# Kernel optimization log

Hardware: AMD Instinct MI355X
Metric: run time of the kernel (lower is better)

The kernel has to match this reference:

```python
import jax, jax.numpy as jnp
import numpy as np

S, B, T, H, E, V, OOV = 400, 16, 64, 512, 256, 50000, 50


def _w(k, shape, scale=0.02):
    return scale * jax.random.normal(k, shape, dtype=jnp.float32)


def setup_inputs() -> dict:
    key = jax.random.key(0)
    ks = jax.random.split(key, 20)
    H2 = H // 2
    return {
        "inputs": jax.random.randint(ks[0], (S, B), 0, V),
        "inputs_length": jnp.full((B,), S, dtype=jnp.int32),  # full lengths (packing is then a no-op)
        "inputs_extended": jax.random.randint(ks[1], (S, B), 0, V + OOV),
        "oov_size": OOV,
        "outputs": jax.random.randint(ks[2], (T, B), 0, V),
        "embedding": _w(ks[3], (V, E)),
        "enc_Wih_f": _w(ks[4], (4 * H2, E)), "enc_Whh_f": _w(ks[5], (4 * H2, H2)),
        "enc_bih_f": jnp.zeros(4 * H2), "enc_bhh_f": jnp.zeros(4 * H2),
        "enc_Wih_b": _w(ks[6], (4 * H2, E)), "enc_Whh_b": _w(ks[7], (4 * H2, H2)),
        "enc_bih_b": jnp.zeros(4 * H2), "enc_bhh_b": jnp.zeros(4 * H2),
        "feat_W": _w(ks[8], (H, H)),
        "dec_Wih": _w(ks[9], (4 * H, E)), "dec_Whh": _w(ks[10], (4 * H, H)),
        "dec_bih": jnp.zeros(4 * H), "dec_bhh": jnp.zeros(4 * H),
        "attn_W": _w(ks[11], (H, H)),
        "vocab_W": _w(ks[12], (V, 3 * H)), "vocab_b": jnp.zeros(V),
        "ptr_W": _w(ks[13], (1, 3 * H)), "ptr_b": jnp.zeros(1),
    }


def _lstm(xs, Wih, Whh, bih, bhh, reverse=False):
    # xs: [S, B, E] -> ys [S, B, H2], final (h, c)
    Bn, H2 = xs.shape[1], Whh.shape[1]

    def step(carry, x):
        h, c = carry
        g = x @ Wih.T + bih + h @ Whh.T + bhh
        i, f, gg, o = jnp.split(g, 4, axis=-1)  # pytorch gate order i,f,g,o
        c = jax.nn.sigmoid(f) * c + jax.nn.sigmoid(i) * jnp.tanh(gg)
        h = jax.nn.sigmoid(o) * jnp.tanh(c)
        return (h, c), h

    init = (jnp.zeros((Bn, H2), xs.dtype), jnp.zeros((Bn, H2), xs.dtype))
    (h, c), ys = jax.lax.scan(step, init, xs, reverse=reverse)
    return ys, h, c


def _forward(inputs, inputs_extended, oov_size, outputs, embedding,
             enc_Wih_f, enc_Whh_f, enc_bih_f, enc_bhh_f,
             enc_Wih_b, enc_Whh_b, enc_bih_b, enc_bhh_b,
             feat_W, dec_Wih, dec_Whh, dec_bih, dec_bhh,
             attn_W, vocab_W, vocab_b, ptr_W, ptr_b):
    Hn = dec_Whh.shape[1]
    Tn, Bn = outputs.shape
    Sn = inputs.shape[0]

    x = embedding[inputs]  # [S,B,E]
    yf, hf, cf = _lstm(x, enc_Wih_f, enc_Whh_f, enc_bih_f, enc_bhh_f)
    yb, hb, cb = _lstm(x, enc_Wih_b, enc_Whh_b, enc_bih_b, enc_bhh_b, reverse=True)
    enc_seq = jnp.concatenate([yf, yb], axis=-1)              # [S,B,H]
    enc_out = jnp.transpose(enc_seq @ feat_W.T, (1, 2, 0))    # Permute(1,2,0) -> [B,H,S]
    # View(-1, H) on [2,B,H/2] stacked states (faithful reshape, incl. batch mixing)
    h0 = jnp.stack([hf, hb]).reshape(-1, Hn)                  # [B,H]
    c0 = jnp.stack([cf, cb]).reshape(-1, Hn)

    yemb = embedding[outputs]                                 # [T,B,E]
    idx = inputs_extended.T                                   # [B,S]
    rows = jnp.arange(Bn)[:, None]
    t_ids = jnp.arange(Tn)

    def step(carry, inp):
        t, xt = inp
        h, c, prev_attn, hid_buf = carry
        # LSTMCell
        g = xt @ dec_Wih.T + dec_bih + h @ dec_Whh.T + dec_bhh
        i, f, gg, o = jnp.split(g, 4, axis=-1)
        c = jax.nn.sigmoid(f) * c + jax.nn.sigmoid(i) * jnp.tanh(gg)
        h = jax.nn.sigmoid(o) * jnp.tanh(c)
        # intra-temporal attention (NB: faithful to source, the *normalized*
        # previous attention is fed back as temporal_scores_sum)
        scores = jnp.exp(jnp.einsum('bh,bhs->bs', h, enc_out))   # [B,S]
        attn = jnp.where(t == 0, scores, scores / prev_attn)
        attn = attn / attn.sum(-1, keepdims=True)                # Normalize(-1)
        enc_ctx = jnp.einsum('bs,bhs->bh', attn, enc_out)        # [B,H]
        # intra-decoder attention over previous decoder hiddens
        keys = hid_buf @ attn_W.T                                # [T,B,H]
        sc = jnp.einsum('bh,tbh->bt', h, keys)
        sc = jnp.where(t_ids[None, :] < t, sc, -1e30)
        a = jax.nn.softmax(sc, axis=-1)
        dec_ctx = jnp.where(t == 0, 0.0, jnp.einsum('bt,tbh->bh', a, hid_buf))
        hid_buf = hid_buf.at[t].set(h)
        # pointer-generator
        feats = jnp.concatenate([h, enc_ctx, dec_ctx], axis=-1)  # [B,3H]
        vdist = jax.nn.softmax(feats @ vocab_W.T + vocab_b, axis=1)
        p = jax.nn.sigmoid(feats @ ptr_W.T + ptr_b)              # [B,1]
        vdist = (1.0 - p) * vdist
        copy = p * attn                                          # [B,S]
        vpad = jnp.pad(vdist, ((0, 0), (0, oov_size)))
        final = vpad.at[rows, idx].add(copy)                     # scatter_add
        return (h, c, attn, hid_buf), final

    hid_buf0 = jnp.zeros((Tn, Bn, Hn))
    init = (h0, c0, jnp.ones((Bn, Sn)), hid_buf0)
    _, preds = jax.lax.scan(step, init, (t_ids, yemb))
    return preds  # [T, B, V+oov]


def reference(inputs, inputs_length, inputs_extended, oov_size, outputs, embedding,
              enc_Wih_f, enc_Whh_f, enc_bih_f, enc_bhh_f,
              enc_Wih_b, enc_Whh_b, enc_bih_b, enc_bhh_b,
              feat_W, dec_Wih, dec_Whh, dec_bih, dec_bhh,
              attn_W, vocab_W, vocab_b, ptr_W, ptr_b):
    # inputs_length is full-length here, so packed RNN == plain scan
    return _forward(inputs, inputs_extended, oov_size, outputs, embedding,
                    enc_Wih_f, enc_Whh_f, enc_bih_f, enc_bhh_f,
                    enc_Wih_b, enc_Whh_b, enc_bih_b, enc_bhh_b,
                    feat_W, dec_Wih, dec_Whh, dec_bih, dec_bhh,
                    attn_W, vocab_W, vocab_b, ptr_W, ptr_b)
```

## Files before the change

### kernel.cpp

```cpp
#include <hip/hip_runtime.h>
#include <cstdint>
#include <cstddef>

typedef unsigned char uchar;
typedef unsigned short ushort;
typedef unsigned int uint;
typedef unsigned long long u64;
typedef __attribute__((ext_vector_type(4))) float f32x4;
typedef __attribute__((ext_vector_type(4))) uint u32x4;
typedef __attribute__((ext_vector_type(4))) int i32x4;

#define DI __device__ __forceinline__

#define S_  400
#define B_  16
#define T_  64
#define H_  512
#define H2_ 256
#define E_  256
#define V_  50000
#define VO_ 50050
#define LP_ 50048

constexpr size_t O_WENCWIH  = 0;
constexpr size_t O_WDECWIH  = O_WENCWIH + (size_t)2048*256*2;
constexpr size_t O_WDECWHH  = O_WDECWIH + (size_t)2048*256*2;
constexpr size_t O_WFEAT    = O_WDECWHH + (size_t)2048*512*2;
constexpr size_t O_WATTN    = O_WFEAT   + (size_t)512*512*2;
constexpr size_t O_BENC     = O_WATTN   + (size_t)512*512*2;
constexpr size_t O_BDEC     = O_BENC    + 2048*4;
constexpr size_t O_WENCWHH8 = O_BDEC    + 2048*4;
constexpr size_t O_XENC     = O_WENCWHH8+ (size_t)2*1024*256;
constexpr size_t O_XDEC     = O_XENC    + (size_t)6400*256*2;
constexpr size_t O_XINENC   = O_XDEC    + (size_t)1024*256*2;
constexpr size_t O_XD       = O_XINENC  + (size_t)2*400*16*1024*2;
constexpr size_t O_ENCSEQ   = O_XD      + (size_t)64*16*2048*2;
constexpr size_t O_ENCOUT   = O_ENCSEQ  + (size_t)6400*512*2;
constexpr size_t O_HFIN     = O_ENCOUT  + (size_t)16*400*512*2;
constexpr size_t O_CFIN     = O_HFIN    + 8192*4;
constexpr size_t O_HBUF     = O_CFIN    + 8192*4;
constexpr size_t O_CSTATE   = O_HBUF    + (size_t)2*8192*2;
constexpr size_t O_HIDBUF   = O_CSTATE  + 8192*4;
constexpr size_t O_KEYS     = O_HIDBUF  + (size_t)64*8192*2;
constexpr size_t O_ATTN     = O_KEYS    + (size_t)64*8192*2;
constexpr size_t O_ATTNQ    = O_ATTN    + (size_t)64*16*400*4;
constexpr size_t O_PSUM     = O_ATTNQ   + (size_t)64*16*400*4;
constexpr size_t O_CTXSLOT  = O_PSUM    + 2*32*16*4;
constexpr size_t O_FEATS    = O_CTXSLOT + (size_t)32*16*512*4;
constexpr size_t O_P        = O_FEATS   + (size_t)1024*1536;
constexpr size_t O_INVSUM   = O_P       + 1024*4;
constexpr size_t O_VOCAB8   = O_INVSUM  + 1024*4;
constexpr size_t O_LOGITS   = O_VOCAB8  + (size_t)50048*1536;
constexpr size_t O_A16      = O_XINENC;
constexpr size_t O_ENCT     = O_A16   + (size_t)16*64*416*2;
constexpr size_t O_HIDT     = O_ENCT  + (size_t)16*512*416*2;

DI float b2f(ushort u){ uint x = ((uint)u) << 16; return __builtin_bit_cast(float, x); }
DI ushort f2b(float f){
  uint u = __builtin_bit_cast(uint, f);
  return (ushort)((u + 0x7fffu + ((u >> 16) & 1u)) >> 16);
}
DI uchar f2e4(float f){
  int q = __builtin_amdgcn_cvt_pk_fp8_f32(f, 0.f, 0, false);
  return (uchar)(q & 0xff);
}
DI uchar f2i8(float f, float scale){
  float q = rintf(f * scale);
  q = fminf(127.f, fmaxf(-127.f, q));
  return (uchar)(signed char)(int)q;
}
DI float e42f(uint b){ return __builtin_amdgcn_cvt_f32_fp8((int)b, 0); }
DI float sigm(float x){ return 1.f / (1.f + __expf(-x)); }
DI float tanhf_(float x){ return 2.f / (1.f + __expf(-2.f * x)) - 1.f; }

DI f32x4 mfma16_bf16(u32x4 a, u32x4 b, f32x4 c){
  asm("v_mfma_f32_16x16x32_bf16 %0, %1, %2, %0" : "+v"(c) : "v"(a), "v"(b));
  return c;
}
DI f32x4 mfma16_fp8(u64 a, u64 b, f32x4 c){
  asm("v_mfma_f32_16x16x32_fp8_fp8 %0, %1, %2, %0" : "+v"(c) : "v"(a), "v"(b));
  return c;
}
DI void mfma_fence(){ asm volatile("s_nop 7\n\ts_nop 7"); }
DI void barrier_lds(){ asm volatile("s_waitcnt lgkmcnt(0)\n\ts_barrier" ::: "memory"); }
DI void wait_vm0(){ asm volatile("s_waitcnt vmcnt(0)" ::: "memory"); }

DI int dot4(int a, int b, int c){
#if __has_builtin(__builtin_amdgcn_sdot4)
  return __builtin_amdgcn_sdot4(a, b, c, false);
#else
  int d;
  asm("v_dot4_i32_i8 %0, %1, %2, %3" : "=v"(d) : "v"(a), "v"(b), "v"(c));
  return d;
#endif
}

typedef __attribute__((address_space(1))) const uchar GU;
typedef __attribute__((address_space(3))) uchar LU;
DI void gload16(const uchar* g, uchar* l){
  __builtin_amdgcn_global_load_lds((GU*)g, (LU*)l, 16, 0, 0);
}

DI float fp8exp4(uint w){
  return __expf(__builtin_amdgcn_cvt_f32_fp8((int)w, 0) * (1.f/1024.f))
       + __expf(__builtin_amdgcn_cvt_f32_fp8((int)w, 1) * (1.f/1024.f))
       + __expf(__builtin_amdgcn_cvt_f32_fp8((int)w, 2) * (1.f/1024.f))
       + __expf(__builtin_amdgcn_cvt_f32_fp8((int)w, 3) * (1.f/1024.f));
}

struct X4 { ushort a, b, c, d; };

__global__ void k_prep(const float* __restrict__ eWf, const float* __restrict__ eWb,
                       const float* __restrict__ dW,  const float* __restrict__ dWhh,
                       const float* __restrict__ fW,  const float* __restrict__ aW,
                       const float* __restrict__ eHf, const float* __restrict__ eHb,
                       const float* __restrict__ bif, const float* __restrict__ bhf,
                       const float* __restrict__ bib, const float* __restrict__ bhb,
                       const float* __restrict__ dbi, const float* __restrict__ dbh,
                       ushort* __restrict__ oEW, ushort* __restrict__ oDW,
                       ushort* __restrict__ oDWhh, ushort* __restrict__ oF,
                       ushort* __restrict__ oA, uchar* __restrict__ oH8,
                       float* __restrict__ oBE, float* __restrict__ oBD){
  const int seg = blockIdx.y;
  const int stride = gridDim.x * 256;
  int n = 262144;
  if (seg == 2) n = 524288;
  else if (seg == 3) n = 1048576;
  else if (seg == 8 || seg == 9) n = 1024;
  else if (seg == 10) n = 2048;
  for (int i = blockIdx.x*256 + threadIdx.x; i < n; i += stride) {
    switch (seg) {
      case 0:  oEW[i]        = f2b(eWf[i]); break;
      case 1:  oEW[262144+i] = f2b(eWb[i]); break;
      case 2:  oDW[i]        = f2b(dW[i]);  break;
      case 3:  oDWhh[i]      = f2b(dWhh[i]);break;
      case 4:  oF[i]         = f2b(fW[i]);  break;
      case 5:  oA[i]         = f2b(aW[i]);  break;
      case 6:  oH8[i]        = f2i8(eHf[i], 1024.f); break;
      case 7:  oH8[262144+i] = f2i8(eHb[i], 1024.f); break;
      case 8:  oBE[i]        = bif[i]+bhf[i]; break;
      case 9:  oBE[1024+i]   = bib[i]+bhb[i]; break;
      case 10: oBD[i]        = dbi[i]+dbh[i]; break;
    }
  }
}

__global__ void k_embed(const int* __restrict__ inp, const int* __restrict__ outp,
                        const float* __restrict__ emb,
                        ushort* __restrict__ xenc, ushort* __restrict__ xdec){
  const int total1 = 6400*32, total2 = 1024*32;
  for (int i = blockIdx.x*256 + threadIdx.x; i < total1 + total2; i += gridDim.x*256) {
    const bool enc = i < total1;
    const int jj = enc ? i : i - total1;
    const int row = jj >> 5, e0 = (jj & 31) << 3;
    const int idx = enc ? inp[row] : outp[row];
    const float4* s4 = (const float4*)(emb + ((size_t)idx << 8) + e0);
    float4 v0 = s4[0], v1 = s4[1];
    uint4 o;
    o.x = (uint)f2b(v0.x) | ((uint)f2b(v0.y) << 16);
    o.y = (uint)f2b(v0.z) | ((uint)f2b(v0.w) << 16);
    o.z = (uint)f2b(v1.x) | ((uint)f2b(v1.y) << 16);
    o.w = (uint)f2b(v1.z) | ((uint)f2b(v1.w) << 16);
    *(uint4*)((enc ? xenc : xdec) + ((size_t)row << 8) + e0) = o;
  }
}

template<int ELSZ, int EPI>
__global__ __launch_bounds__(256)
void k_gemm(const uchar* __restrict__ A, const uchar* __restrict__ Bm,
            int mtiles, int kbytes, int arow, int brow,
            uchar* __restrict__ dst, const float* __restrict__ bias){
  __shared__ __align__(16) uchar sm[32768];
  const int tid = threadIdx.x;
  int bx = blockIdx.x;
  if ((gridDim.x & 7) == 0) {
    const int nb = gridDim.x >> 3;
    bx = (bx & 7) * nb + (bx >> 3);
  }
  const int mt = bx % mtiles, nt = bx / mtiles;
  const int m0 = mt << 7, n0 = nt << 7;
  const int w = tid >> 6, l = tid & 63, lr = l & 15, lh = l >> 4;
  const int wr = w >> 1, wc = w & 1;

  f32x4 acc[4][4];
#pragma unroll
  for (int i = 0; i < 4; ++i)
#pragma unroll
    for (int j = 0; j < 4; ++j) { f32x4 z = {0.f,0.f,0.f,0.f}; acc[i][j] = z; }

  const int iters = kbytes >> 6;
  const int roff = tid << 4;
  const int r0 = roff >> 6, c0 = roff & 63;
  const uchar* pa0 = A  + (size_t)(m0 + r0)      * arow + c0;
  const uchar* pa1 = A  + (size_t)(m0 + r0 + 64) * arow + c0;
  const uchar* pb0 = Bm + (size_t)(n0 + r0)      * brow + c0;
  const uchar* pb1 = Bm + (size_t)(n0 + r0 + 64) * brow + c0;

  auto issue = [&](int kt){
    const int ko = kt << 6;
    uchar* db = sm + ((kt & 1) << 14);
    gload16(pa0 + ko, db + roff);
    gload16(pa1 + ko, db + 4096 + roff);
    gload16(pb0 + ko, db + 8192 + roff);
    gload16(pb1 + ko, db + 12288 + roff);
  };

  issue(0);
  wait_vm0();
  __syncthreads();

  for (int kt = 0; kt < iters; ++kt) {
    if (kt + 1 < iters) issue(kt + 1);
    const uchar* smc = sm + ((kt & 1) << 14);
    if constexpr (ELSZ == 2) {
      u32x4 af[4], bf[4];
#pragma unroll
      for (int i = 0; i < 4; ++i) af[i] = *(const u32x4*)(smc + ((wr<<6)+(i<<4)+lr)*64 + (lh<<4));
#pragma unroll
      for (int j = 0; j < 4; ++j) bf[j] = *(const u32x4*)(smc + 8192 + ((wc<<6)+(j<<4)+lr)*64 + (lh<<4));
#pragma unroll
      for (int i = 0; i < 4; ++i)
#pragma unroll
        for (int j = 0; j < 4; ++j) acc[i][j] = mfma16_bf16(af[i], bf[j], acc[i][j]);
    } else {
#pragma unroll
      for (int kk = 0; kk < 2; ++kk) {
        u64 af[4], bf[4];
#pragma unroll
        for (int i = 0; i < 4; ++i) af[i] = *(const u64*)(smc + ((wr<<6)+(i<<4)+lr)*64 + (kk<<5) + (lh<<3));
#pragma unroll
        for (int j = 0; j < 4; ++j) bf[j] = *(const u64*)(smc + 8192 + ((wc<<6)+(j<<4)+lr)*64 + (kk<<5) + (lh<<3));
#pragma unroll
        for (int i = 0; i < 4; ++i)
#pragma unroll
          for (int j = 0; j < 4; ++j) acc[i][j] = mfma16_fp8(af[i], bf[j], acc[i][j]);
      }
    }
    wait_vm0();
    __syncthreads();
  }
  mfma_fence();

  if constexpr (EPI == 0 || EPI == 1) {
#pragma unroll
    for (int j = 0; j < 4; ++j) {
      const int n = n0 + (wc<<6) + (j<<4) + lr;
      const float bz = bias[n];
#pragma unroll
      for (int i = 0; i < 4; ++i)
#pragma unroll
        for (int r = 0; r < 4; ++r) {
          const int m = m0 + (wr<<6) + (i<<4) + (lh<<2) + r;
          const float v = acc[i][j][r] + bz;
          size_t addr;
          if constexpr (EPI == 0) {
            addr = ((size_t)((n >> 10)*6400 + m) << 10) + (n & 1023);
          } else {
            addr = ((size_t)m << 11) + n;
          }
          ((ushort*)dst)[addr] = f2b(v);
        }
    }
  } else if constexpr (EPI == 4) {
#pragma unroll
    for (int j = 0; j < 4; ++j) {
      const int n = n0 + (wc<<6) + (j<<4) + lr;
#pragma unroll
      for (int i = 0; i < 4; ++i)
#pragma unroll
        for (int r = 0; r < 4; ++r) {
          const int m = m0 + (wr<<6)+(i<<4)+(lh<<2)+r;
          ((ushort*)dst)[ ((size_t)m << 9) + n ] = f2b(acc[i][j][r]);
        }
    }
  } else {
    __syncthreads();
#pragma unroll
    for (int j = 0; j < 4; ++j) {
      const int nl = (wc<<6) + (j<<4) + lr;
      const int n = n0 + nl;
      const float bz = (n < V_) ? bias[n] : 0.f;
#pragma unroll
      for (int i = 0; i < 4; ++i)
#pragma unroll
        for (int r = 0; r < 4; ++r) {
          const int ml = (wr<<6)+(i<<4)+(lh<<2)+r;
          const float v = acc[i][j][r] * (1.f/2048.f) + bz;
          sm[ml*128 + nl] = f2e4(v * 1024.f);
        }
    }
    __syncthreads();
    const int row = tid >> 1, half = tid & 1;
    const uchar* srow = sm + row*128 + (half<<6);
    uchar* grow = dst + (size_t)(m0 + row) * LP_ + n0 + (half<<6);
#pragma unroll
    for (int cc4 = 0; cc4 < 4; ++cc4) {
      const int n = n0 + (half<<6) + (cc4<<4);
      if (n + 16 <= V_) {
        *(uint4*)(grow + (cc4<<4)) = *(const uint4*)(srow + (cc4<<4));
      } else {
        for (int bb = 0; bb < 16; ++bb) if (n + bb < V_) grow[(cc4<<4)+bb] = srow[(cc4<<4)+bb];
      }
    }
  }
}

__global__ __launch_bounds__(256)
void k_tr(const ushort* __restrict__ enc, ushort* __restrict__ encT){
  const int bid = blockIdx.x;
  const int b = bid / 20, rem = bid % 20;
  const int sc = rem >> 2, hc = rem & 3;
  const int s0 = sc*80, h0 = hc << 7;
  __shared__ ushort tl[80*130];
  const int t = threadIdx.x;
#pragma unroll
  for (int i = 0; i < 40; ++i) {
    const int idx = t + i*256;
    const int hh = idx & 127, si = idx >> 7;
    tl[si*130 + hh] = enc[ ((size_t)(((s0+si)<<4) + b) << 9) + h0 + hh ];
  }
  __syncthreads();
#pragma unroll
  for (int i = 0; i < 40; ++i) {
    const int idx = t + i*256;
    const int ss = idx % 80, hh = idx / 80;
    encT[ ((size_t)((b<<9) + h0 + hh))*416 + s0 + ss ] = tl[ss*130 + hh];
  }
}

__global__ __launch_bounds__(1024)
void k_encoder(const ushort* __restrict__ Xin, const uchar* __restrict__ Whh8,
               ushort* __restrict__ encseq, float* __restrict__ hfin, float* __restrict__ cfin,
               const float* __restrict__ vocabW, uchar* __restrict__ vocab8){
  const int bid = blockIdx.x;
  const int tid = threadIdx.x;
  if (bid >= 32) {
    const int n4 = 19200000, ntot4 = 19218432;
    const int stride = (gridDim.x - 32) * 1024;
    for (int i = (bid - 32)*1024 + tid; i < ntot4; i += stride) {
      uint o = 0;
      if (i < n4) {
        const float4 v = *(const float4*)(vocabW + (size_t)i*4);
        int lo = __builtin_amdgcn_cvt_pk_fp8_f32(v.x*16.f, v.y*16.f, 0, false);
        int hi = __builtin_amdgcn_cvt_pk_fp8_f32(v.z*16.f, v.w*16.f, 0, false);
        o = ((uint)lo & 0xffffu) | ((uint)hi << 16);
      }
      *(uint*)(vocab8 + (size_t)i*4) = o;
    }
    return;
  }
  const int d = bid >> 4, bglob = bid & 15;
  __shared__ __align__(16) uchar hl[2][256];
  __shared__ float gl[1024];
  if (tid < 128) ((uint*)hl)[tid] = 0;
  u32x4 wf[16];
  const uchar* Wr = Whh8 + ((size_t)d << 18) + ((size_t)tid << 8);
#pragma unroll
  for (int j = 0; j < 16; ++j) wf[j] = *(const u32x4*)(Wr + (j << 4));
  const int u = tid & 255;
  float cc = 0.f;
  const ushort* xin_base = Xin + ((size_t)(d*6400) << 10);

  auto xld = [&](int s) -> X4 {
    const int t = d ? 399 - s : s;
    const ushort* p = xin_base + (((size_t)(t*16 + bglob)) << 10) + u;
    X4 r; r.a = p[0]; r.b = p[256]; r.c = p[512]; r.d = p[768];
    return r;
  };

  auto STEP = [&](int s, X4 xv) {
    const int cur = s & 1;
    const u32x4* hp = (const u32x4*)&hl[cur][0];
    int a0 = 0, a1 = 0, a2 = 0, a3 = 0;
#pragma unroll
    for (int j = 0; j < 16; ++j) {
      const u32x4 h4 = hp[j];
      a0 = dot4((int)h4[0], (int)wf[j][0], a0);
      a1 = dot4((int)h4[1], (int)wf[j][1], a1);
      a2 = dot4((int)h4[2], (int)wf[j][2], a2);
      a3 = dot4((int)h4[3], (int)wf[j][3], a3);
    }
    gl[tid] = (float)((a0 + a1) + (a2 + a3));
    barrier_lds();
    if (tid < 256) {
      const int t = d ? 399 - s : s;
      const float gi = b2f(xv.a) + gl[u]      *(1.f/8388608.f);
      const float gf = b2f(xv.b) + gl[256+u]  *(1.f/8388608.f);
      const float gg = b2f(xv.c) + gl[512+u]  *(1.f/8388608.f);
      const float go = b2f(xv.d) + gl[768+u]  *(1.f/8388608.f);
      cc = sigm(gf)*cc + sigm(gi)*tanhf_(gg);
      const float h = sigm(go)*tanhf_(cc);
      encseq[ ((size_t)((t<<4) + bglob) << 9) + (d<<8) + u ] = f2b(h);
      hl[cur^1][u] = f2i8(h, 8192.f);
      if (s == 399) {
        hfin[ (((d<<4)+bglob) << 8) + u ] = h;
        cfin[ (((d<<4)+bglob) << 8) + u ] = cc;
      }
    }
    barrier_lds();
  };

  X4 xv0 = {0,0,0,0};
  if (tid < 256) xv0 = xld(0);
  barrier_lds();
  for (int s = 0; s < 400; s += 2) {
    X4 xv1 = {0,0,0,0};
    if (tid < 256) xv1 = xld(s + 1);
    STEP(s, xv0);
    if (tid < 256) xv0 = xld(s + 2 <= 399 ? s + 2 : 399);
    STEP(s + 1, xv1);
  }
}

__global__ void k_h0z(const float* __restrict__ hfin, const float* __restrict__ cfin,
                      ushort* __restrict__ hbuf, float* __restrict__ cstate,
                      ushort* __restrict__ encT){
  const int tid = blockIdx.x*256 + threadIdx.x;
  if (tid < 8192) {
    const int r = tid >> 9, ch = tid & 511;
    const int d = r >> 3, b = ((r & 7) << 1) + (ch >> 8), u = ch & 255;
    const int src = (((d<<4)+b) << 8) + u;
    hbuf[8192 + tid] = f2b(hfin[src]);
    cstate[tid] = cfin[src];
  }
  if (tid < 16*512*16) {
    const int b = tid >> 13, h = (tid >> 4) & 511, sp = tid & 15;
    encT[((size_t)((b<<9) + h))*416 + 400 + sp] = 0;
  }
}

__global__ __launch_bounds__(256)
void k_lstm(int t, const ushort* __restrict__ Xd, const ushort* __restrict__ Whh,
            ushort* __restrict__ hbuf, float* __restrict__ cstate,
            ushort* __restrict__ hidbuf, ushort* __restrict__ hidT,
            uchar* __restrict__ feats){
  const int q = blockIdx.x, tid = threadIdx.x;
  const int w = tid >> 6, l = tid & 63, lr = l & 15, lh = l >> 4;
  __shared__ float gl[4][16][16];
  const ushort* hprev = hbuf + (((t+1)&1) << 13);
  f32x4 acc = {0.f,0.f,0.f,0.f};
  const ushort* Wrow = Whh + ((size_t)((w<<9) + (q<<4) + lr) << 9);
#pragma unroll
  for (int kk = 0; kk < 16; ++kk) {
    u32x4 a = *(const u32x4*)(hprev + (lr<<9) + (kk<<5) + (lh<<3));
    u32x4 b = *(const u32x4*)(Wrow + (kk<<5) + (lh<<3));
    acc = mfma16_bf16(a, b, acc);
  }
  mfma_fence();
#pragma unroll
  for (int r = 0; r < 4; ++r) {
    const int b = (lh<<2) + r;
    const float xvv = b2f(Xd[ ((size_t)((t<<4)+b) << 11) + (w<<9) + (q<<4) + lr ]);
    gl[w][b][lr] = acc[r] + xvv;
  }
  __syncthreads();
  const int b = tid >> 4, ul = tid & 15, uu = (q<<4) + ul;
  const float gi = gl[0][b][ul], gf = gl[1][b][ul], gg = gl[2][b][ul], go = gl[3][b][ul];
  float cc = cstate[(b<<9) + uu];
  cc = sigm(gf)*cc + sigm(gi)*tanhf_(gg);
  const float h = sigm(go)*tanhf_(cc);
  cstate[(b<<9)+uu] = cc;
  const ushort hb16 = f2b(h);
  hbuf[((t&1)<<13) + (b<<9) + uu] = hb16;
  hidbuf[((size_t)t<<13) + (b<<9) + uu] = hb16;
  hidT[((size_t)((b<<9)+uu) << 6) + t] = hb16;
  feats[(size_t)((t<<4)+b)*1536 + uu] = f2e4(h*128.f);
}

__global__ __launch_bounds__(256)
void k_score(const ushort* __restrict__ hid, const ushort* __restrict__ enc,
             float* __restrict__ E){
  const int b = blockIdx.x / 5, nc = blockIdx.x % 5;
  const int w = threadIdx.x >> 6, l = threadIdx.x & 63, lr = l & 15, lh = l >> 4;
  f32x4 acc[5];
#pragma unroll
  for (int j = 0; j < 5; ++j) { f32x4 z = {0.f,0.f,0.f,0.f}; acc[j] = z; }
#pragma unroll 4
  for (int kk = 0; kk < 16; ++kk) {
    const u32x4 a = *(const u32x4*)(hid + ((size_t)(((w<<4)+lr)<<4 | b) << 9) + (kk<<5) + (lh<<3));
#pragma unroll
    for (int j = 0; j < 5; ++j) {
      const int s = nc*80 + j*16 + lr;
      const u32x4 bb = *(const u32x4*)(enc + ((size_t)((s<<4) + b) << 9) + (kk<<5) + (lh<<3));
      acc[j] = mfma16_bf16(a, bb, acc[j]);
    }
  }
  mfma_fence();
#pragma unroll
  for (int j = 0; j < 5; ++j)
#pragma unroll
    for (int r = 0; r < 4; ++r) {
      const int t = (w<<4) + (lh<<2) + r;
      const int s = nc*80 + j*16 + lr;
      E[ ((size_t)(t*16 + b))*400 + s ] = __expf(acc[j][r]);
    }
}

__global__ __launch_bounds__(256)
void k_tnorm(const float* __restrict__ E, float* __restrict__ attnB,
             ushort* __restrict__ a16){
  const int b = blockIdx.x, tid = threadIdx.x;
  const int s0 = tid, s1 = tid + 256;
  __shared__ float red[4];
  __shared__ float bcv, qsv;
  float qp0 = 1.f, qp1 = 1.f, qsp = 1.f;
  for (int t = 0; t < 64; ++t) {
    const float e0 = E[ ((size_t)(t*16 + b))*400 + s0 ];
    const float e1 = (s1 < 400) ? E[ ((size_t)(t*16 + b))*400 + s1 ] : 0.f;
    const float q0 = t ? e0 * qsp / qp0 : e0;
    const float q1 = (s1 < 400) ? (t ? e1 * qsp / qp1 : e1) : 0.f;
    qp0 = q0; if (s1 < 400) qp1 = q1;
    float ss = q0 + q1;
#pragma unroll
    for (int off = 32; off > 0; off >>= 1) ss += __shfl_down(ss, off, 64);
    if ((tid & 63) == 0) red[tid >> 6] = ss;
    __syncthreads();
    if (tid == 0) {
      const float tot = red[0] + red[1] + red[2] + red[3];
      qsv = tot; bcv = 1.f / tot;
    }
    __syncthreads();
    const float inv = bcv;
    attnB[ ((size_t)(t*16 + b))*400 + s0 ] = q0 * inv;
    a16[ ((size_t)(b*64 + t))*416 + s0 ] = f2b(q0 * inv);
    if (s1 < 416) {
      if (s1 < 400) attnB[ ((size_t)(t*16 + b))*400 + s1 ] = q1 * inv;
      a16[ ((size_t)(b*64 + t))*416 + s1 ] = (s1 < 400) ? f2b(q1 * inv) : (ushort)0;
    }
    qsp = qsv;
    __syncthreads();
  }
}

__global__ __launch_bounds__(256)
void k_ctx(const ushort* __restrict__ a16, const ushort* __restrict__ encT,
           uchar* __restrict__ feats){
  const int b = blockIdx.x;
  const int w = threadIdx.x >> 6, l = threadIdx.x & 63, lr = l & 15, lh = l >> 4;
  f32x4 acc[4][8];
#pragma unroll
  for (int i = 0; i < 4; ++i)
#pragma unroll
    for (int j = 0; j < 8; ++j) { f32x4 z = {0.f,0.f,0.f,0.f}; acc[i][j] = z; }
  for (int kk = 0; kk < 13; ++kk) {
    u32x4 a[4];
#pragma unroll
    for (int mf = 0; mf < 4; ++mf)
      a[mf] = *(const u32x4*)(a16 + ((size_t)(b*64 + (mf<<4)+lr))*416 + (kk<<5) + (lh<<3));
#pragma unroll
    for (int j = 0; j < 8; ++j) {
      const int h = ((w<<3)+j)*16 + lr;
      const u32x4 bb = *(const u32x4*)(encT + ((size_t)((b<<9)+h))*416 + (kk<<5) + (lh<<3));
#pragma unroll
      for (int mf = 0; mf < 4; ++mf) acc[mf][j] = mfma16_bf16(a[mf], bb, acc[mf][j]);
    }
  }
  mfma_fence();
#pragma unroll
  for (int mf = 0; mf < 4; ++mf)
#pragma unroll
    for (int j = 0; j < 8; ++j)
#pragma unroll
      for (int r = 0; r < 4; ++r) {
        const int t = (mf<<4) + (lh<<2) + r;
        const int h = ((w<<3)+j)*16 + lr;
        feats[ (size_t)((t<<4)+b)*1536 + 512 + h ] = f2e4(acc[mf][j][r] * 128.f);
      }
}

__global__ __launch_bounds__(256)
void k_dattn(const ushort* __restrict__ hid, const ushort* __restrict__ keys,
             const ushort* __restrict__ hidT, uchar* __restrict__ feats){
  const int b = blockIdx.x;
  const int tid = threadIdx.x;
  const int w = tid >> 6, l = tid & 63, lr = l & 15, lh = l >> 4;
  __shared__ float sc[64*65];
  __shared__ ushort pb[64*72];
  {
    f32x4 acc[4];
#pragma unroll
    for (int i = 0; i < 4; ++i) { f32x4 z = {0.f,0.f,0.f,0.f}; acc[i] = z; }
#pragma unroll 4
    for (int kk = 0; kk < 16; ++kk) {
      const u32x4 bb = *(const u32x4*)(keys + ((size_t)((((w<<4)+lr)<<4) + b) << 9) + (kk<<5) + (lh<<3));
#pragma unroll
      for (int mf = 0; mf < 4; ++mf) {
        const u32x4 a = *(const u32x4*)(hid + ((size_t)((((mf<<4)+lr)<<4) + b) << 9) + (kk<<5) + (lh<<3));
        acc[mf] = mfma16_bf16(a, bb, acc[mf]);
      }
    }
    mfma_fence();
#pragma unroll
    for (int mf = 0; mf < 4; ++mf)
#pragma unroll
      for (int r = 0; r < 4; ++r)
        sc[ ((mf<<4)+(lh<<2)+r)*65 + (w<<4)+lr ] = acc[mf][r];
  }
  __syncthreads();
  for (int rr = 0; rr < 16; ++rr) {
    const int row = (w<<4) + rr;
    const float v = sc[row*65 + l];
    const bool act = l < row;
    float vm = act ? v : -3.0e38f;
    float m = vm;
#pragma unroll
    for (int off = 32; off > 0; off >>= 1) m = fmaxf(m, __shfl_xor(m, off, 64));
    const float e = act ? __expf(vm - m) : 0.f;
    float ssum = e;
#pragma unroll
    for (int off = 32; off > 0; off >>= 1) ssum += __shfl_xor(ssum, off, 64);
    const float p = (row == 0) ? 0.f : e / ssum;
    pb[row*72 + l] = f2b(p);
  }
  __syncthreads();
  {
    f32x4 acc[4][8];
#pragma unroll
    for (int i = 0; i < 4; ++i)
#pragma unroll
      for (int j = 0; j < 8; ++j) { f32x4 z = {0.f,0.f,0.f,0.f}; acc[i][j] = z; }
#pragma unroll
    for (int kk = 0; kk < 2; ++kk) {
      u32x4 a[4];
#pragma unroll
      for (int mf = 0; mf < 4; ++mf)
        a[mf] = *(const u32x4*)&pb[ ((mf<<4)+lr)*72 + (kk<<5) + (lh<<3) ];
#pragma unroll
      for (int j = 0; j < 8; ++j) {
        const int h = ((w<<3)+j)*16 + lr;
        const u32x4 bb = *(const u32x4*)(hidT + ((size_t)((b<<9)+h) << 6) + (kk<<5) + (lh<<3));
#pragma unroll
        for (int mf = 0; mf < 4; ++mf) acc[mf][j] = mfma16_bf16(a[mf], bb, acc[mf][j]);
      }
    }
    mfma_fence();
#pragma unroll
    for (int mf = 0; mf < 4; ++mf)
#pragma unroll
      for (int j = 0; j < 8; ++j)
#pragma unroll
        for (int r = 0; r < 4; ++r) {
          const int t = (mf<<4) + (lh<<2) + r;
          const int h = ((w<<3)+j)*16 + lr;
          feats[ (size_t)((t<<4)+b)*1536 + 1024 + h ] = f2e4(acc[mf][j][r] * 128.f);
        }
  }
}

__global__ __launch_bounds__(256)
void k_final2(const uchar* __restrict__ logits, const uchar* __restrict__ feats,
              const float* __restrict__ ptrW, const float* __restrict__ ptrb,
              const float* __restrict__ attnB, const int* __restrict__ iext,
              float* __restrict__ out){
  const int row = blockIdx.x, tid = threadIdx.x;
  const uchar* lrow = logits + (size_t)row * LP_;
  float s = 0.f;
  for (int c = tid*16; c < V_; c += 4096) {
    const uint4 v = *(const uint4*)(lrow + c);
    s += fp8exp4(v.x) + fp8exp4(v.y) + fp8exp4(v.z) + fp8exp4(v.w);
  }
  const uchar* f = feats + (size_t)row*1536;
  float pd = 0.f;
  for (int k = tid*4; k < 1536; k += 1024) {
    const uint wv = *(const uint*)(f + k);
    pd += __builtin_amdgcn_cvt_f32_fp8((int)wv,0)*ptrW[k]
        + __builtin_amdgcn_cvt_f32_fp8((int)wv,1)*ptrW[k+1]
        + __builtin_amdgcn_cvt_f32_fp8((int)wv,2)*ptrW[k+2]
        + __builtin_amdgcn_cvt_f32_fp8((int)wv,3)*ptrW[k+3];
  }
#pragma unroll
  for (int off = 32; off > 0; off >>= 1) {
    s  += __shfl_down(s,  off, 64);
    pd += __shfl_down(pd, off, 64);
  }
  __shared__ float wsum[4], wpd[4];
  __shared__ float oms, pvs;
  if ((tid & 63) == 0) { wsum[tid>>6] = s; wpd[tid>>6] = pd; }
  __syncthreads();
  if (tid == 0) {
    const float pv = sigm((wpd[0]+wpd[1]+wpd[2]+wpd[3]) * (1.f/128.f) + ptrb[0]);
    pvs = pv;
    oms = (1.f - pv) / (wsum[0]+wsum[1]+wsum[2]+wsum[3]);
  }
  __syncthreads();
  const float om = oms;
  float* orow = out + (size_t)row * VO_;
  for (int v = tid; v < VO_; v += 256) {
    float val = 0.f;
    if (v < V_) val = om * __expf(e42f((uint)lrow[v]) * (1.f/1024.f));
    orow[v] = val;
  }
  __syncthreads();
  const float pv = pvs;
  const int b = row & 15;
  const float* arow = attnB + (size_t)row*400;
  for (int sidx = tid; sidx < 400; sidx += 256) {
    atomicAdd(orow + iext[sidx*16 + b], pv * arow[sidx]);
  }
}

extern "C" void kernel_launch(void* const* d_in, const int* in_sizes, int n_in,
                              void* d_out, int out_size, void* d_ws, size_t ws_size,
                              hipStream_t stream){
  (void)in_sizes; (void)n_in; (void)out_size; (void)ws_size;
  const int*   inputs     = (const int*)  d_in[0];
  const int*   inputs_ext = (const int*)  d_in[2];
  const int*   outputs    = (const int*)  d_in[4];
  const float* embedding  = (const float*)d_in[5];
  const float* enc_Wih_f  = (const float*)d_in[6];
  const float* enc_Whh_f  = (const float*)d_in[7];
  const float* enc_bih_f  = (const float*)d_in[8];
  const float* enc_bhh_f  = (const float*)d_in[9];
  const float* enc_Wih_b  = (const float*)d_in[10];
  const float* enc_Whh_b  = (const float*)d_in[11];
  const float* enc_bih_b  = (const float*)d_in[12];
  const float* enc_bhh_b  = (const float*)d_in[13];
  const float* feat_W     = (const float*)d_in[14];
  const float* dec_Wih    = (const float*)d_in[15];
  const float* dec_Whh    = (const float*)d_in[16];
  const float* dec_bih    = (const float*)d_in[17];
  const float* dec_bhh    = (const float*)d_in[18];
  const float* attn_W     = (const float*)d_in[19];
  const float* vocab_W    = (const float*)d_in[20];
  const float* vocab_b    = (const float*)d_in[21];
  const float* ptr_W      = (const float*)d_in[22];
  const float* ptr_b      = (const float*)d_in[23];

  uchar* W = (uchar*)d_ws;
  ushort* wEncWih  = (ushort*)(W + O_WENCWIH);
  ushort* wDecWih  = (ushort*)(W + O_WDECWIH);
  ushort* wDecWhh  = (ushort*)(W + O_WDECWHH);
  ushort* wFeat    = (ushort*)(W + O_WFEAT);
  ushort* wAttn    = (ushort*)(W + O_WATTN);
  float*  bEnc     = (float*) (W + O_BENC);
  float*  bDec     = (float*) (W + O_BDEC);
  uchar*  wEncWhh8 = (uchar*) (W + O_WENCWHH8);
  ushort* xEnc     = (ushort*)(W + O_XENC);
  ushort* xDec     = (ushort*)(W + O_XDEC);
  ushort* XinEnc   = (ushort*)(W + O_XINENC);
  ushort* Xd       = (ushort*)(W + O_XD);
  ushort* encSeq   = (ushort*)(W + O_ENCSEQ);
  ushort* encOut   = (ushort*)(W + O_ENCOUT);
  float*  hFin     = (float*) (W + O_HFIN);
  float*  cFin     = (float*) (W + O_CFIN);
  ushort* hBuf     = (ushort*)(W + O_HBUF);
  float*  cState   = (float*) (W + O_CSTATE);
  ushort* hidBuf   = (ushort*)(W + O_HIDBUF);
  ushort* keys     = (ushort*)(W + O_KEYS);
  float*  attnB    = (float*) (W + O_ATTN);
  float*  Ebuf     = (float*) (W + O_ATTNQ);
  ushort* a16      = (ushort*)(W + O_A16);
  ushort* encT     = (ushort*)(W + O_ENCT);
  ushort* hidT     = (ushort*)(W + O_HIDT);
  uchar*  feats    = (uchar*) (W + O_FEATS);
  uchar*  vocab8   = (uchar*) (W + O_VOCAB8);
  uchar*  logits   = (uchar*) (W + O_LOGITS);
  float*  out      = (float*) d_out;

  k_prep<<<dim3(96, 11), 256, 0, stream>>>(enc_Wih_f, enc_Wih_b, dec_Wih, dec_Whh, feat_W, attn_W,
                                           enc_Whh_f, enc_Whh_b, enc_bih_f, enc_bhh_f,
                                           enc_bih_b, enc_bhh_b, dec_bih, dec_bhh,
                                           wEncWih, wDecWih, wDecWhh, wFeat, wAttn,
                                           wEncWhh8, bEnc, bDec);

  k_embed<<<928, 256, 0, stream>>>(inputs, outputs, embedding, xEnc, xDec);

  k_gemm<2,0><<<50*16, 256, 0, stream>>>((const uchar*)xEnc, (const uchar*)wEncWih,
                                         50, 512, 512, 512, (uchar*)XinEnc, bEnc);
  k_gemm<2,1><<<8*16, 256, 0, stream>>>((const uchar*)xDec, (const uchar*)wDecWih,
                                        8, 512, 512, 512, (uchar*)Xd, bDec);

  k_encoder<<<256, 1024, 0, stream>>>(XinEnc, wEncWhh8, encSeq, hFin, cFin, vocab_W, vocab8);
  k_h0z<<<512, 256, 0, stream>>>(hFin, cFin, hBuf, cState, encT);

  k_gemm<2,4><<<50*4, 256, 0, stream>>>((const uchar*)encSeq, (const uchar*)wFeat,
                                        50, 1024, 1024, 1024, (uchar*)encOut, nullptr);
  k_tr<<<320, 256, 0, stream>>>(encOut, encT);

  for (int t = 0; t < T_; ++t) {
    k_lstm<<<32, 256, 0, stream>>>(t, Xd, wDecWhh, hBuf, cState, hidBuf, hidT, feats);
  }

  k_gemm<2,4><<<8*4, 256, 0, stream>>>((const uchar*)hidBuf, (const uchar*)wAttn,
                                       8, 1024, 1024, 1024, (uchar*)keys, nullptr);
  k_score<<<80, 256, 0, stream>>>(hidBuf, encOut, Ebuf);
  k_tnorm<<<16, 256, 0, stream>>>(Ebuf, attnB, a16);
  k_ctx<<<16, 256, 0, stream>>>(a16, encT, feats);
  k_dattn<<<16, 256, 0, stream>>>(hidBuf, keys, hidT, feats);

  k_gemm<1,3><<<8*391, 256, 0, stream>>>(feats, vocab8, 8, 1536, 1536, 1536, logits, vocab_b);

  k_final2<<<1024, 256, 0, stream>>>(logits, feats, ptr_W, ptr_b, attnB, inputs_ext, out);
}
```

Baseline: 1.469 ms.

## Give each encoder thread all four gates and broadcast h via readlane

```diff
diff --git a/kernel.cpp b/kernel.cpp
--- a/kernel.cpp
+++ b/kernel.cpp
@@ -328,7 +328,7 @@
   }
 }
 
-__global__ __launch_bounds__(1024)
+__global__ __launch_bounds__(256, 1)
 void k_encoder(const ushort* __restrict__ Xin, const uchar* __restrict__ Whh8,
                ushort* __restrict__ encseq, float* __restrict__ hfin, float* __restrict__ cfin,
                const float* __restrict__ vocabW, uchar* __restrict__ vocab8){
@@ -337,27 +337,37 @@
   if (bid >= 32) {
     const int n4 = 19200000, ntot4 = 19218432;
     const int stride = (gridDim.x - 32) * 1024;
-    for (int i = (bid - 32)*1024 + tid; i < ntot4; i += stride) {
-      uint o = 0;
-      if (i < n4) {
-        const float4 v = *(const float4*)(vocabW + (size_t)i*4);
-        int lo = __builtin_amdgcn_cvt_pk_fp8_f32(v.x*16.f, v.y*16.f, 0, false);
-        int hi = __builtin_amdgcn_cvt_pk_fp8_f32(v.z*16.f, v.w*16.f, 0, false);
-        o = ((uint)lo & 0xffffu) | ((uint)hi << 16);
+    for (int i0 = (bid - 32)*1024 + tid; i0 < ntot4; i0 += stride) {
+      float4 v[4];
+#pragma unroll
+      for (int k = 0; k < 4; ++k) {
+        const int i = i0 + k*256;
+        if (i < n4) v[k] = *(const float4*)(vocabW + (size_t)i*4);
+        else { v[k].x = 0.f; v[k].y = 0.f; v[k].z = 0.f; v[k].w = 0.f; }
       }
-      *(uint*)(vocab8 + (size_t)i*4) = o;
+#pragma unroll
+      for (int k = 0; k < 4; ++k) {
+        const int i = i0 + k*256;
+        if (i < ntot4) {
+          int lo = __builtin_amdgcn_cvt_pk_fp8_f32(v[k].x*16.f, v[k].y*16.f, 0, false);
+          int hi = __builtin_amdgcn_cvt_pk_fp8_f32(v[k].z*16.f, v[k].w*16.f, 0, false);
+          *(uint*)(vocab8 + (size_t)i*4) = ((uint)lo & 0xffffu) | ((uint)hi << 16);
+        }
+      }
     }
     return;
   }
   const int d = bid >> 4, bglob = bid & 15;
   __shared__ __align__(16) uchar hl[2][256];
-  __shared__ float gl[1024];
   if (tid < 128) ((uint*)hl)[tid] = 0;
-  u32x4 wf[16];
-  const uchar* Wr = Whh8 + ((size_t)d << 18) + ((size_t)tid << 8);
-#pragma unroll
-  for (int j = 0; j < 16; ++j) wf[j] = *(const u32x4*)(Wr + (j << 4));
-  const int u = tid & 255;
+  u32x4 wf[4][16];
+#pragma unroll
+  for (int g = 0; g < 4; ++g) {
+    const uchar* Wr = Whh8 + ((size_t)d << 18) + (((size_t)((g<<8) + tid)) << 8);
+#pragma unroll
+    for (int j = 0; j < 16; ++j) wf[g][j] = *(const u32x4*)(Wr + (j << 4));
+  }
+  const int u = tid;
   float cc = 0.f;
   const ushort* xin_base = Xin + ((size_t)(d*6400) << 10);
 
@@ -368,46 +378,42 @@
     return r;
   };
 
+  barrier_lds();
+  uint vh = ((const uint*)hl[0])[tid & 63];
+
   auto STEP = [&](int s, X4 xv) {
-    const int cur = s & 1;
-    const u32x4* hp = (const u32x4*)&hl[cur][0];
     int a0 = 0, a1 = 0, a2 = 0, a3 = 0;
 #pragma unroll
-    for (int j = 0; j < 16; ++j) {
-      const u32x4 h4 = hp[j];
-      a0 = dot4((int)h4[0], (int)wf[j][0], a0);
-      a1 = dot4((int)h4[1], (int)wf[j][1], a1);
-      a2 = dot4((int)h4[2], (int)wf[j][2], a2);
-      a3 = dot4((int)h4[3], (int)wf[j][3], a3);
-    }
-    gl[tid] = (float)((a0 + a1) + (a2 + a3));
+    for (int j = 0; j < 64; ++j) {
+      const int hw = (int)__builtin_amdgcn_readlane(vh, j);
+      a0 = dot4(hw, (int)wf[0][j>>2][j&3], a0);
+      a1 = dot4(hw, (int)wf[1][j>>2][j&3], a1);
+      a2 = dot4(hw, (int)wf[2][j>>2][j&3], a2);
+      a3 = dot4(hw, (int)wf[3][j>>2][j&3], a3);
+    }
+    const int t = d ? 399 - s : s;
+    const float gi = b2f(xv.a) + (float)a0*(1.f/8388608.f);
+    const float gf = b2f(xv.b) + (float)a1*(1.f/8388608.f);
+    const float gg = b2f(xv.c) + (float)a2*(1.f/8388608.f);
+    const float go = b2f(xv.d) + (float)a3*(1.f/8388608.f);
+    cc = sigm(gf)*cc + sigm(gi)*tanhf_(gg);
+    const float h = sigm(go)*tanhf_(cc);
+    encseq[ ((size_t)((t<<4) + bglob) << 9) + (d<<8) + u ] = f2b(h);
+    const int nb = (s + 1) & 1;
+    hl[nb][u] = f2i8(h, 8192.f);
+    if (s == 399) {
+      hfin[ (((d<<4)+bglob) << 8) + u ] = h;
+      cfin[ (((d<<4)+bglob) << 8) + u ] = cc;
+    }
     barrier_lds();
-    if (tid < 256) {
-      const int t = d ? 399 - s : s;
-      const float gi = b2f(xv.a) + gl[u]      *(1.f/8388608.f);
-      const float gf = b2f(xv.b) + gl[256+u]  *(1.f/8388608.f);
-      const float gg = b2f(xv.c) + gl[512+u]  *(1.f/8388608.f);
-      const float go = b2f(xv.d) + gl[768+u]  *(1.f/8388608.f);
-      cc = sigm(gf)*cc + sigm(gi)*tanhf_(gg);
-      const float h = sigm(go)*tanhf_(cc);
-      encseq[ ((size_t)((t<<4) + bglob) << 9) + (d<<8) + u ] = f2b(h);
-      hl[cur^1][u] = f2i8(h, 8192.f);
-      if (s == 399) {
-        hfin[ (((d<<4)+bglob) << 8) + u ] = h;
-        cfin[ (((d<<4)+bglob) << 8) + u ] = cc;
-      }
-    }
-    barrier_lds();
+    vh = ((const uint*)hl[nb])[tid & 63];
   };
 
-  X4 xv0 = {0,0,0,0};
-  if (tid < 256) xv0 = xld(0);
-  barrier_lds();
+  X4 xv0 = xld(0);
   for (int s = 0; s < 400; s += 2) {
-    X4 xv1 = {0,0,0,0};
-    if (tid < 256) xv1 = xld(s + 1);
+    X4 xv1 = xld(s + 1);
     STEP(s, xv0);
-    if (tid < 256) xv0 = xld(s + 2 <= 399 ? s + 2 : 399);
+    xv0 = xld(s + 2 <= 399 ? s + 2 : 399);
     STEP(s + 1, xv1);
   }
 }
@@ -770,7 +776,7 @@
   k_gemm<2,1><<<8*16, 256, 0, stream>>>((const uchar*)xDec, (const uchar*)wDecWih,
                                         8, 512, 512, 512, (uchar*)Xd, bDec);
 
-  k_encoder<<<256, 1024, 0, stream>>>(XinEnc, wEncWhh8, encSeq, hFin, cFin, vocab_W, vocab8);
+  k_encoder<<<256, 256, 0, stream>>>(XinEnc, wEncWhh8, encSeq, hFin, cFin, vocab_W, vocab8);
   k_h0z<<<512, 256, 0, stream>>>(hFin, cFin, hBuf, cState, encT);
 
   k_gemm<2,4><<<50*4, 256, 0, stream>>>((const uchar*)encSeq, (const uchar*)wFeat,
```

Measured after the change: 1.545 ms. +5.2%, slower.
